# Kernel optimization log

Hardware: AMD Instinct MI355X
Metric: run time of the kernel (lower is better)

Reference implementation:

```python
import jax, jax.numpy as jnp
import numpy as np

N_HEAD = 16
K_SPARSE = 16

def setup_inputs() -> dict:
    key = jax.random.key(0)
    k1, k2, k3, k4 = jax.random.split(key, 4)
    B, T, C = 4, 1024, 1024
    x = jax.random.normal(k1, (B, T, C), dtype=jnp.float32)
    W_attn = jax.random.normal(k2, (3 * C, C), dtype=jnp.float32) * 0.02
    W_proj = jax.random.normal(k3, (C, C), dtype=jnp.float32) * 0.02
    W_rel = jax.random.normal(k4, (N_HEAD, C), dtype=jnp.float32) * 0.02
    return {"x": x, "W_attn": W_attn, "W_proj": W_proj, "W_rel": W_rel}


def reference(x, W_attn, W_proj, W_rel):
    B, T, C = x.shape
    H = W_rel.shape[0]
    hd = C // H
    K = min(K_SPARSE, T)

    # qkv projection (no bias): [B,T,3C] -> three [B,H,T,hd]
    qkv = x @ W_attn.T
    q, k, v = jnp.split(qkv, 3, axis=-1)
    q = q.reshape(B, T, H, hd).transpose(0, 2, 1, 3)
    k = k.reshape(B, T, H, hd).transpose(0, 2, 1, 3)
    v = v.reshape(B, T, H, hd).transpose(0, 2, 1, 3)

    # per-head relevance scores of batch 0 (original indexes top_indices[0]),
    # masked with row 0 of the causal tril (original uses masked_relevance[:, 0, :]):
    # only position 0 keeps a finite score.
    rel = jnp.einsum('tc,hc->ht', x[0], W_rel)              # [H,T]
    s = jnp.where(jnp.arange(T) == 0, rel, -jnp.inf)         # [H,T]

    t_ar = jnp.arange(T)
    # per-query masking (j <= t) then top-k routing per (head, t)
    scores = jnp.where(t_ar[:, None] >= t_ar[None, :], s[:, None, :], -jnp.inf)  # [H,T,T]
    _, idx = jax.lax.top_k(scores, K)                        # [H,T,K]
    slots = jnp.arange(K)
    # for t+1 <= K the original uses arange(t+1) (valid slots masked below)
    idx = jnp.where((t_ar < K)[None, :, None], slots[None, None, :], idx)
    valid = slots[None, :] <= t_ar[:, None]                  # [T,K]

    # gather selected keys / values: [B,H,T,K,hd]
    h_ix = jnp.arange(H)[:, None, None]
    k_sel = k[:, h_ix, idx]
    v_sel = v[:, h_ix, idx]

    logits = jnp.einsum('bhtd,bhtkd->bhtk', q, k_sel) / jnp.sqrt(jnp.float32(hd))
    logits = jnp.where(valid[None, None], logits, -jnp.inf)
    w = jax.nn.softmax(logits, axis=-1)                      # dropout = identity (eval)
    out = jnp.einsum('bhtk,bhtkd->bhtd', w, v_sel)

    out = out.transpose(0, 2, 1, 3).reshape(B, T, C)
    return out @ W_proj.T
```

## Files before the change

kernel.cpp:

```cpp
#include <hip/hip_runtime.h>
#include <hip/hip_bf16.h>
#include <stdint.h>

typedef __bf16 bf16x8 __attribute__((ext_vector_type(8)));
typedef float  f32x4  __attribute__((ext_vector_type(4)));

constexpr int Bb = 4;
constexpr int Tt = 1024;
constexpr int Cc = 1024;
constexpr int Kk = 16;
constexpr int HK = 256;
constexpr int KSPL = 8;

__device__ inline __bf16 f2bf(float f) {
    union { __hip_bfloat16 h; __bf16 b; } u;
    u.h = __float2bfloat16(f);
    return u.b;
}

__device__ inline void load_lds16(const void* g, void* l) {
    auto gp = (const __attribute__((address_space(1))) unsigned int*)(uintptr_t)g;
    auto lp = (__attribute__((address_space(3))) unsigned int*)(uintptr_t)l;
    __builtin_amdgcn_global_load_lds(gp, lp, 16, 0, 0);
}

__device__ inline bf16x8 cvt8(const float* p) {
    f32x4 lo = *reinterpret_cast<const f32x4*>(p);
    f32x4 hi = *reinterpret_cast<const f32x4*>(p + 4);
    bf16x8 r;
    r[0] = f2bf(lo[0]); r[1] = f2bf(lo[1]); r[2] = f2bf(lo[2]); r[3] = f2bf(lo[3]);
    r[4] = f2bf(hi[0]); r[5] = f2bf(hi[1]); r[6] = f2bf(hi[2]); r[7] = f2bf(hi[3]);
    return r;
}

__global__ __launch_bounds__(256)
void kv_gemm(const float* __restrict__ x, const float* __restrict__ Wkv,
             float* __restrict__ kv_part, __hip_bfloat16* __restrict__ xb)
{
    __shared__ __hip_bfloat16 As[64 * 40];
    __shared__ __hip_bfloat16 Bs[64 * 40];
    const int tid = threadIdx.x;

    if (blockIdx.z >= KSPL) {
        const int cb = (blockIdx.z - KSPL) * 32 + blockIdx.x;
        const size_t base = (size_t)cb * 16384;
#pragma unroll
        for (int i = 0; i < 8; ++i) {
            size_t off = base + (size_t)(i * 256 + tid) * 8;
            *reinterpret_cast<bf16x8*>(xb + off) = cvt8(x + off);
        }
        return;
    }

    const int lane = tid & 63;
    const int wave = tid >> 6;
    const int wm = wave >> 1, wn = wave & 1;
    const int tileN = blockIdx.x * 64;
    const int kz = blockIdx.z;
    const int r16 = lane & 15;
    const int kq  = (lane >> 4) * 8;

    const int sr = tid >> 2, sc = (tid & 3) * 8;
    const size_t arow = (size_t)(sr >> 4) * Tt + (sr & 15);

    f32x4 acc[2][2] = {};
    for (int kk = kz * 128; kk < kz * 128 + 128; kk += 32) {
        *reinterpret_cast<bf16x8*>(As + sr * 40 + sc) = cvt8(x + arow * Cc + kk + sc);
        *reinterpret_cast<bf16x8*>(Bs + sr * 40 + sc) = cvt8(Wkv + (size_t)(tileN + sr) * Cc + kk + sc);
        __syncthreads();
        bf16x8 a[2], b[2];
#pragma unroll
        for (int i = 0; i < 2; ++i) {
            a[i] = *reinterpret_cast<const bf16x8*>(As + (wm * 32 + i * 16 + r16) * 40 + kq);
            b[i] = *reinterpret_cast<const bf16x8*>(Bs + (wn * 32 + i * 16 + r16) * 40 + kq);
        }
#pragma unroll
        for (int i = 0; i < 2; ++i)
#pragma unroll
            for (int j = 0; j < 2; ++j)
                acc[i][j] = __builtin_amdgcn_mfma_f32_16x16x32_bf16(a[i], b[j], acc[i][j], 0, 0, 0);
        __syncthreads();
    }

    const int crow0 = (lane >> 4) * 4;
    const int ccol  = lane & 15;
    float* outp = kv_part + (size_t)kz * 64 * 2048;
#pragma unroll
    for (int i = 0; i < 2; ++i)
#pragma unroll
        for (int j = 0; j < 2; ++j)
#pragma unroll
            for (int r = 0; r < 4; ++r)
                outp[(size_t)(wm * 32 + i * 16 + crow0 + r) * 2048
                     + tileN + wn * 32 + j * 16 + ccol] = acc[i][j][r];
}

__global__ __launch_bounds__(256)
void precompute(const float* __restrict__ kv_part,
                const float* __restrict__ W_attn,
                const float* __restrict__ W_proj,
                __hip_bfloat16* __restrict__ QKb,
                __hip_bfloat16* __restrict__ vPt)
{
    __shared__ float sel[64][16];
    const int blk = blockIdx.x;
    const int type = blk >> 8;
    const int bh = (blk >> 2) & 63;
    const int cchunk = blk & 3;
    const int b = bh >> 4, h = bh & 15;
    const int tid = threadIdx.x;

    for (int e = tid; e < Kk * 64; e += 256) {
        int k = e >> 6, d = e & 63;
        size_t off = (size_t)(b * Kk + k) * 2048 + type * 1024 + h * 64 + d;
        float s = 0.f;
#pragma unroll
        for (int p = 0; p < KSPL; ++p) s += kv_part[off + (size_t)p * 64 * 2048];
        sel[d][k] = s;
    }
    __syncthreads();

    const int c = cchunk * 256 + tid;
    float acc[Kk] = {};

    if (type == 0) {
        const float* wp = W_attn + (size_t)(h * 64) * 1024 + c;
#pragma unroll 8
        for (int d = 0; d < 64; ++d) {
            float wv = wp[(size_t)d * 1024];
            const float4* sv = reinterpret_cast<const float4*>(sel[d]);
            float4 s0 = sv[0], s1 = sv[1], s2 = sv[2], s3 = sv[3];
            acc[0]  += wv * s0.x; acc[1]  += wv * s0.y; acc[2]  += wv * s0.z; acc[3]  += wv * s0.w;
            acc[4]  += wv * s1.x; acc[5]  += wv * s1.y; acc[6]  += wv * s1.z; acc[7]  += wv * s1.w;
            acc[8]  += wv * s2.x; acc[9]  += wv * s2.y; acc[10] += wv * s2.z; acc[11] += wv * s2.w;
            acc[12] += wv * s3.x; acc[13] += wv * s3.y; acc[14] += wv * s3.z; acc[15] += wv * s3.w;
        }
#pragma unroll
        for (int k = 0; k < Kk; ++k)
            QKb[((size_t)b * HK + h * 16 + k) * 1024 + c] = __float2bfloat16(acc[k]);
    } else {
        const float* wrow = W_proj + (size_t)c * 1024 + h * 64;
#pragma unroll 8
        for (int d4 = 0; d4 < 64; d4 += 4) {
            float4 wv = *reinterpret_cast<const float4*>(wrow + d4);
            const float w4[4] = {wv.x, wv.y, wv.z, wv.w};
#pragma unroll
            for (int dd = 0; dd < 4; ++dd) {
                float wvv = w4[dd];
                const float4* sv = reinterpret_cast<const float4*>(sel[d4 + dd]);
                float4 s0 = sv[0], s1 = sv[1], s2 = sv[2], s3 = sv[3];
                acc[0]  += wvv * s0.x; acc[1]  += wvv * s0.y; acc[2]  += wvv * s0.z; acc[3]  += wvv * s0.w;
                acc[4]  += wvv * s1.x; acc[5]  += wvv * s1.y; acc[6]  += wvv * s1.z; acc[7]  += wvv * s1.w;
                acc[8]  += wvv * s2.x; acc[9]  += wvv * s2.y; acc[10] += wvv * s2.z; acc[11] += wvv * s2.w;
                acc[12] += wvv * s3.x; acc[13] += wvv * s3.y; acc[14] += wvv * s3.z; acc[15] += wvv * s3.w;
            }
        }
        bf16x8 p0, p1;
#pragma unroll
        for (int k = 0; k < 8; ++k) { p0[k] = f2bf(acc[k]); p1[k] = f2bf(acc[k + 8]); }
        __hip_bfloat16* dst = vPt + ((size_t)b * 1024 + c) * HK + h * 16;
        *reinterpret_cast<bf16x8*>(dst) = p0;
        *reinterpret_cast<bf16x8*>(dst + 8) = p1;
    }
}

__global__ __launch_bounds__(256)
void logits_softmax(const __hip_bfloat16* __restrict__ xb,
                    const __hip_bfloat16* __restrict__ QKb,
                    __hip_bfloat16* __restrict__ wout)
{
    __shared__ __hip_bfloat16 Ah[4][32 * 32];
    __shared__ __hip_bfloat16 Bh[4][64 * 32];

    const __hip_bfloat16* A = xb + (size_t)blockIdx.z * Tt * Cc;
    const __hip_bfloat16* Bm = QKb + (size_t)blockIdx.z * HK * Cc;

    const int tid = threadIdx.x;
    const int lane = tid & 63;
    const int wave = tid >> 6;
    const int wm = wave >> 1, wn = wave & 1;
    const int tileM = blockIdx.y * 32;
    const int tileN = blockIdx.x * 64;
    const int r16 = lane & 15;
    const int kq  = (lane >> 4) * 8;

    f32x4 acc[2] = {};
    for (int kk = 0; kk < Cc; kk += 128) {
        {
            int g = wave * 64 + lane;
#pragma unroll
            for (int s = 0; s < 4; ++s)
                load_lds16(Bm + (size_t)(tileN + (g >> 2)) * Cc + kk + s * 32 + (g & 3) * 8,
                           &Bh[s][0] + wave * 512);
#pragma unroll
            for (int h = 0; h < 2; ++h)
                load_lds16(A + (size_t)(tileM + h * 16 + (lane >> 2)) * Cc + kk + wave * 32 + (lane & 3) * 8,
                           &Ah[wave][0] + h * 512);
        }
        __syncthreads();

#pragma unroll
        for (int s = 0; s < 4; ++s) {
            bf16x8 a = *reinterpret_cast<const bf16x8*>(&Ah[s][0] + (wm * 16 + r16) * 32 + kq);
#pragma unroll
            for (int j = 0; j < 2; ++j) {
                bf16x8 b = *reinterpret_cast<const bf16x8*>(
                    &Bh[s][0] + (wn * 32 + j * 16 + r16) * 32 + kq);
                acc[j] = __builtin_amdgcn_mfma_f32_16x16x32_bf16(a, b, acc[j], 0, 0, 0);
            }
        }
        __syncthreads();
    }

    const int crow0 = (lane >> 4) * 4;
    const int ccol  = lane & 15;
#pragma unroll
    for (int r = 0; r < 4; ++r) {
        int t = tileM + wm * 16 + crow0 + r;
        bool valid = (ccol <= t);
#pragma unroll
        for (int j = 0; j < 2; ++j) {
            int hk = tileN + wn * 32 + j * 16 + ccol;
            float v = acc[j][r] * 0.125f;
            float vm = valid ? v : -3.0e38f;
#pragma unroll
            for (int m = 1; m < 16; m <<= 1) vm = fmaxf(vm, __shfl_xor(vm, m));
            float e = valid ? __expf(v - vm) : 0.f;
            float s = e;
#pragma unroll
            for (int m = 1; m < 16; m <<= 1) s += __shfl_xor(s, m);
            wout[((size_t)blockIdx.z * Tt + t) * HK + hk] = __float2bfloat16(e / s);
        }
    }
}

__global__ __launch_bounds__(256)
void out_gemm(const __hip_bfloat16* __restrict__ Aw,
              const __hip_bfloat16* __restrict__ Bv,
              float* __restrict__ Cout)
{
    __shared__ __hip_bfloat16 As[2][64 * 32];
    __shared__ __hip_bfloat16 Bs[2][64 * 32];

    const __hip_bfloat16* A = Aw + (size_t)blockIdx.z * Tt * HK;
    const __hip_bfloat16* Bm = Bv + (size_t)blockIdx.z * Cc * HK;

    const int lane = threadIdx.x & 63;
    const int wave = threadIdx.x >> 6;
    const int wm = wave >> 1, wn = wave & 1;
    const int tileM = blockIdx.y * 64;
    const int tileN = blockIdx.x * 64;
    const int r16 = lane & 15;
    const int kq  = (lane >> 4) * 8;

    f32x4 acc[2][2] = {};
    for (int kk = 0; kk < HK; kk += 64) {
        {
            int g = wave * 64 + lane;
#pragma unroll
            for (int s = 0; s < 2; ++s) {
                load_lds16(A + (size_t)(tileM + (g >> 2)) * HK + kk + s * 32 + (g & 3) * 8,
                           &As[s][0] + wave * 512);
                load_lds16(Bm + (size_t)(tileN + (g >> 2)) * HK + kk + s * 32 + (g & 3) * 8,
                           &Bs[s][0] + wave * 512);
            }
        }
        __syncthreads();
#pragma unroll
        for (int s = 0; s < 2; ++s) {
            bf16x8 a[2], b[2];
#pragma unroll
            for (int i = 0; i < 2; ++i) {
                a[i] = *reinterpret_cast<const bf16x8*>(&As[s][0] + (wm * 32 + i * 16 + r16) * 32 + kq);
                b[i] = *reinterpret_cast<const bf16x8*>(&Bs[s][0] + (wn * 32 + i * 16 + r16) * 32 + kq);
            }
#pragma unroll
            for (int i = 0; i < 2; ++i)
#pragma unroll
                for (int j = 0; j < 2; ++j)
                    acc[i][j] = __builtin_amdgcn_mfma_f32_16x16x32_bf16(a[i], b[j], acc[i][j], 0, 0, 0);
        }
        __syncthreads();
    }

    const int crow0 = (lane >> 4) * 4;
    const int ccol  = lane & 15;
    float* outp = Cout + (size_t)blockIdx.z * Tt * Cc;
#pragma unroll
    for (int i = 0; i < 2; ++i)
#pragma unroll
        for (int j = 0; j < 2; ++j)
#pragma unroll
            for (int r = 0; r < 4; ++r)
                outp[(size_t)(tileM + wm * 32 + i * 16 + crow0 + r) * Cc
                     + tileN + wn * 32 + j * 16 + ccol] = acc[i][j][r];
}

extern "C" void kernel_launch(void* const* d_in, const int* in_sizes, int n_in,
                              void* d_out, int out_size, void* d_ws, size_t ws_size,
                              hipStream_t stream)
{
    (void)in_sizes; (void)n_in; (void)out_size; (void)ws_size;
    const float* x      = (const float*)d_in[0];
    const float* W_attn = (const float*)d_in[1];
    const float* W_proj = (const float*)d_in[2];
    float* out = (float*)d_out;

    char* ws = (char*)d_ws;
    float*          kv_part = (float*)ws;
    __hip_bfloat16* QKb  = (__hip_bfloat16*)(ws + (4u << 20));
    __hip_bfloat16* vPt  = (__hip_bfloat16*)(ws + (6u << 20));
    __hip_bfloat16* w_ws = (__hip_bfloat16*)(ws + (8u << 20));
    __hip_bfloat16* xb   = (__hip_bfloat16*)(ws + (10u << 20));

    kv_gemm<<<dim3(32, 1, 2 * KSPL), 256, 0, stream>>>(x, W_attn + (size_t)Cc * Cc, kv_part, xb);
    precompute<<<512, 256, 0, stream>>>(kv_part, W_attn, W_proj, QKb, vPt);
    logits_softmax<<<dim3(HK / 64, Tt / 32, Bb), 256, 0, stream>>>(xb, QKb, w_ws);
    out_gemm<<<dim3(16, 16, Bb), 256, 0, stream>>>(w_ws, vPt, out);
}
```

Before: 114.9 us.

## Fuse four kernels into one persistent kernel with global grid barriers

Merges the kv GEMM, precompute, logits/softmax and output GEMM launches into a single 512-block kernel separated by atomic spin-wait grid barriers. The output GEMM stage now handles two tiles per block to fit the fixed grid. This removes per-launch overhead and inter-kernel gaps, at the cost of a memset for the barrier counters and reliance on all 512 blocks being co-resident; if they are not, the spin-wait can hang or time out.

New measurement: 252.8 us. 2.2x slower.

```diff
diff --git a/kernel.cpp b/kernel.cpp
--- a/kernel.cpp
+++ b/kernel.cpp
@@ -11,6 +11,7 @@
 constexpr int Kk = 16;
 constexpr int HK = 256;
 constexpr int KSPL = 8;
+constexpr unsigned NBLK = 512;
 
 __device__ inline __bf16 f2bf(float f) {
     union { __hip_bfloat16 h; __bf16 b; } u;
@@ -33,267 +34,281 @@
     return r;
 }
 
-__global__ __launch_bounds__(256)
-void kv_gemm(const float* __restrict__ x, const float* __restrict__ Wkv,
-             float* __restrict__ kv_part, __hip_bfloat16* __restrict__ xb)
+__device__ inline void grid_sync(unsigned* cnt) {
+    __syncthreads();
+    if (threadIdx.x == 0) {
+        __hip_atomic_fetch_add(cnt, 1u, __ATOMIC_ACQ_REL, __HIP_MEMORY_SCOPE_AGENT);
+        unsigned spins = 0;
+        while (__hip_atomic_load(cnt, __ATOMIC_ACQUIRE, __HIP_MEMORY_SCOPE_AGENT) < NBLK
+               && ++spins < (1u << 30)) {
+            __builtin_amdgcn_s_sleep(2);
+        }
+    }
+    __syncthreads();
+}
+
+__global__ __launch_bounds__(256, 2)
+void fused_all(const float* __restrict__ x,
+               const float* __restrict__ W_attn,
+               const float* __restrict__ W_proj,
+               float* __restrict__ kv_part,
+               __hip_bfloat16* __restrict__ QKb,
+               __hip_bfloat16* __restrict__ vPt,
+               __hip_bfloat16* __restrict__ w_ws,
+               __hip_bfloat16* __restrict__ xb,
+               float* __restrict__ out,
+               unsigned* __restrict__ bar)
 {
-    __shared__ __hip_bfloat16 As[64 * 40];
-    __shared__ __hip_bfloat16 Bs[64 * 40];
-    const int tid = threadIdx.x;
-
-    if (blockIdx.z >= KSPL) {
-        const int cb = (blockIdx.z - KSPL) * 32 + blockIdx.x;
+    __shared__ __align__(16) char smem[24576];
+
+    const int tid  = threadIdx.x;
+    const int lane = tid & 63;
+    const int wave = tid >> 6;
+    const int blk  = blockIdx.x;
+
+    if (blk >= 256) {
+        const int cb = blk - 256;
         const size_t base = (size_t)cb * 16384;
 #pragma unroll
         for (int i = 0; i < 8; ++i) {
             size_t off = base + (size_t)(i * 256 + tid) * 8;
             *reinterpret_cast<bf16x8*>(xb + off) = cvt8(x + off);
         }
-        return;
-    }
-
-    const int lane = tid & 63;
-    const int wave = tid >> 6;
-    const int wm = wave >> 1, wn = wave & 1;
-    const int tileN = blockIdx.x * 64;
-    const int kz = blockIdx.z;
-    const int r16 = lane & 15;
-    const int kq  = (lane >> 4) * 8;
-
-    const int sr = tid >> 2, sc = (tid & 3) * 8;
-    const size_t arow = (size_t)(sr >> 4) * Tt + (sr & 15);
-
-    f32x4 acc[2][2] = {};
-    for (int kk = kz * 128; kk < kz * 128 + 128; kk += 32) {
-        *reinterpret_cast<bf16x8*>(As + sr * 40 + sc) = cvt8(x + arow * Cc + kk + sc);
-        *reinterpret_cast<bf16x8*>(Bs + sr * 40 + sc) = cvt8(Wkv + (size_t)(tileN + sr) * Cc + kk + sc);
-        __syncthreads();
-        bf16x8 a[2], b[2];
-#pragma unroll
-        for (int i = 0; i < 2; ++i) {
-            a[i] = *reinterpret_cast<const bf16x8*>(As + (wm * 32 + i * 16 + r16) * 40 + kq);
-            b[i] = *reinterpret_cast<const bf16x8*>(Bs + (wn * 32 + i * 16 + r16) * 40 + kq);
-        }
-#pragma unroll
-        for (int i = 0; i < 2; ++i)
-#pragma unroll
-            for (int j = 0; j < 2; ++j)
-                acc[i][j] = __builtin_amdgcn_mfma_f32_16x16x32_bf16(a[i], b[j], acc[i][j], 0, 0, 0);
-        __syncthreads();
-    }
-
-    const int crow0 = (lane >> 4) * 4;
-    const int ccol  = lane & 15;
-    float* outp = kv_part + (size_t)kz * 64 * 2048;
-#pragma unroll
-    for (int i = 0; i < 2; ++i)
-#pragma unroll
-        for (int j = 0; j < 2; ++j)
-#pragma unroll
-            for (int r = 0; r < 4; ++r)
-                outp[(size_t)(wm * 32 + i * 16 + crow0 + r) * 2048
-                     + tileN + wn * 32 + j * 16 + ccol] = acc[i][j][r];
-}
-
-__global__ __launch_bounds__(256)
-void precompute(const float* __restrict__ kv_part,
-                const float* __restrict__ W_attn,
-                const float* __restrict__ W_proj,
-                __hip_bfloat16* __restrict__ QKb,
-                __hip_bfloat16* __restrict__ vPt)
-{
-    __shared__ float sel[64][16];
-    const int blk = blockIdx.x;
-    const int type = blk >> 8;
-    const int bh = (blk >> 2) & 63;
-    const int cchunk = blk & 3;
-    const int b = bh >> 4, h = bh & 15;
-    const int tid = threadIdx.x;
-
-    for (int e = tid; e < Kk * 64; e += 256) {
-        int k = e >> 6, d = e & 63;
-        size_t off = (size_t)(b * Kk + k) * 2048 + type * 1024 + h * 64 + d;
-        float s = 0.f;
-#pragma unroll
-        for (int p = 0; p < KSPL; ++p) s += kv_part[off + (size_t)p * 64 * 2048];
-        sel[d][k] = s;
-    }
-    __syncthreads();
-
-    const int c = cchunk * 256 + tid;
-    float acc[Kk] = {};
-
-    if (type == 0) {
-        const float* wp = W_attn + (size_t)(h * 64) * 1024 + c;
-#pragma unroll 8
-        for (int d = 0; d < 64; ++d) {
-            float wv = wp[(size_t)d * 1024];
-            const float4* sv = reinterpret_cast<const float4*>(sel[d]);
-            float4 s0 = sv[0], s1 = sv[1], s2 = sv[2], s3 = sv[3];
-            acc[0]  += wv * s0.x; acc[1]  += wv * s0.y; acc[2]  += wv * s0.z; acc[3]  += wv * s0.w;
-            acc[4]  += wv * s1.x; acc[5]  += wv * s1.y; acc[6]  += wv * s1.z; acc[7]  += wv * s1.w;
-            acc[8]  += wv * s2.x; acc[9]  += wv * s2.y; acc[10] += wv * s2.z; acc[11] += wv * s2.w;
-            acc[12] += wv * s3.x; acc[13] += wv * s3.y; acc[14] += wv * s3.z; acc[15] += wv * s3.w;
-        }
-#pragma unroll
-        for (int k = 0; k < Kk; ++k)
-            QKb[((size_t)b * HK + h * 16 + k) * 1024 + c] = __float2bfloat16(acc[k]);
     } else {
-        const float* wrow = W_proj + (size_t)c * 1024 + h * 64;
-#pragma unroll 8
-        for (int d4 = 0; d4 < 64; d4 += 4) {
-            float4 wv = *reinterpret_cast<const float4*>(wrow + d4);
-            const float w4[4] = {wv.x, wv.y, wv.z, wv.w};
-#pragma unroll
-            for (int dd = 0; dd < 4; ++dd) {
-                float wvv = w4[dd];
-                const float4* sv = reinterpret_cast<const float4*>(sel[d4 + dd]);
-                float4 s0 = sv[0], s1 = sv[1], s2 = sv[2], s3 = sv[3];
-                acc[0]  += wvv * s0.x; acc[1]  += wvv * s0.y; acc[2]  += wvv * s0.z; acc[3]  += wvv * s0.w;
-                acc[4]  += wvv * s1.x; acc[5]  += wvv * s1.y; acc[6]  += wvv * s1.z; acc[7]  += wvv * s1.w;
-                acc[8]  += wvv * s2.x; acc[9]  += wvv * s2.y; acc[10] += wvv * s2.z; acc[11] += wvv * s2.w;
-                acc[12] += wvv * s3.x; acc[13] += wvv * s3.y; acc[14] += wvv * s3.z; acc[15] += wvv * s3.w;
-            }
-        }
-        bf16x8 p0, p1;
-#pragma unroll
-        for (int k = 0; k < 8; ++k) { p0[k] = f2bf(acc[k]); p1[k] = f2bf(acc[k + 8]); }
-        __hip_bfloat16* dst = vPt + ((size_t)b * 1024 + c) * HK + h * 16;
-        *reinterpret_cast<bf16x8*>(dst) = p0;
-        *reinterpret_cast<bf16x8*>(dst + 8) = p1;
-    }
-}
-
-__global__ __launch_bounds__(256)
-void logits_softmax(const __hip_bfloat16* __restrict__ xb,
-                    const __hip_bfloat16* __restrict__ QKb,
-                    __hip_bfloat16* __restrict__ wout)
-{
-    __shared__ __hip_bfloat16 Ah[4][32 * 32];
-    __shared__ __hip_bfloat16 Bh[4][64 * 32];
-
-    const __hip_bfloat16* A = xb + (size_t)blockIdx.z * Tt * Cc;
-    const __hip_bfloat16* Bm = QKb + (size_t)blockIdx.z * HK * Cc;
-
-    const int tid = threadIdx.x;
-    const int lane = tid & 63;
-    const int wave = tid >> 6;
-    const int wm = wave >> 1, wn = wave & 1;
-    const int tileM = blockIdx.y * 32;
-    const int tileN = blockIdx.x * 64;
-    const int r16 = lane & 15;
-    const int kq  = (lane >> 4) * 8;
-
-    f32x4 acc[2] = {};
-    for (int kk = 0; kk < Cc; kk += 128) {
-        {
-            int g = wave * 64 + lane;
-#pragma unroll
-            for (int s = 0; s < 4; ++s)
-                load_lds16(Bm + (size_t)(tileN + (g >> 2)) * Cc + kk + s * 32 + (g & 3) * 8,
-                           &Bh[s][0] + wave * 512);
-#pragma unroll
-            for (int h = 0; h < 2; ++h)
-                load_lds16(A + (size_t)(tileM + h * 16 + (lane >> 2)) * Cc + kk + wave * 32 + (lane & 3) * 8,
-                           &Ah[wave][0] + h * 512);
-        }
-        __syncthreads();
-
-#pragma unroll
-        for (int s = 0; s < 4; ++s) {
-            bf16x8 a = *reinterpret_cast<const bf16x8*>(&Ah[s][0] + (wm * 16 + r16) * 32 + kq);
-#pragma unroll
-            for (int j = 0; j < 2; ++j) {
-                bf16x8 b = *reinterpret_cast<const bf16x8*>(
-                    &Bh[s][0] + (wn * 32 + j * 16 + r16) * 32 + kq);
-                acc[j] = __builtin_amdgcn_mfma_f32_16x16x32_bf16(a, b, acc[j], 0, 0, 0);
-            }
-        }
-        __syncthreads();
-    }
-
-    const int crow0 = (lane >> 4) * 4;
-    const int ccol  = lane & 15;
-#pragma unroll
-    for (int r = 0; r < 4; ++r) {
-        int t = tileM + wm * 16 + crow0 + r;
-        bool valid = (ccol <= t);
-#pragma unroll
-        for (int j = 0; j < 2; ++j) {
-            int hk = tileN + wn * 32 + j * 16 + ccol;
-            float v = acc[j][r] * 0.125f;
-            float vm = valid ? v : -3.0e38f;
-#pragma unroll
-            for (int m = 1; m < 16; m <<= 1) vm = fmaxf(vm, __shfl_xor(vm, m));
-            float e = valid ? __expf(v - vm) : 0.f;
-            float s = e;
-#pragma unroll
-            for (int m = 1; m < 16; m <<= 1) s += __shfl_xor(s, m);
-            wout[((size_t)blockIdx.z * Tt + t) * HK + hk] = __float2bfloat16(e / s);
-        }
-    }
-}
-
-__global__ __launch_bounds__(256)
-void out_gemm(const __hip_bfloat16* __restrict__ Aw,
-              const __hip_bfloat16* __restrict__ Bv,
-              float* __restrict__ Cout)
-{
-    __shared__ __hip_bfloat16 As[2][64 * 32];
-    __shared__ __hip_bfloat16 Bs[2][64 * 32];
-
-    const __hip_bfloat16* A = Aw + (size_t)blockIdx.z * Tt * HK;
-    const __hip_bfloat16* Bm = Bv + (size_t)blockIdx.z * Cc * HK;
-
-    const int lane = threadIdx.x & 63;
-    const int wave = threadIdx.x >> 6;
-    const int wm = wave >> 1, wn = wave & 1;
-    const int tileM = blockIdx.y * 64;
-    const int tileN = blockIdx.x * 64;
-    const int r16 = lane & 15;
-    const int kq  = (lane >> 4) * 8;
-
-    f32x4 acc[2][2] = {};
-    for (int kk = 0; kk < HK; kk += 64) {
-        {
-            int g = wave * 64 + lane;
-#pragma unroll
-            for (int s = 0; s < 2; ++s) {
-                load_lds16(A + (size_t)(tileM + (g >> 2)) * HK + kk + s * 32 + (g & 3) * 8,
-                           &As[s][0] + wave * 512);
-                load_lds16(Bm + (size_t)(tileN + (g >> 2)) * HK + kk + s * 32 + (g & 3) * 8,
-                           &Bs[s][0] + wave * 512);
-            }
-        }
-        __syncthreads();
-#pragma unroll
-        for (int s = 0; s < 2; ++s) {
+        const float* Wkv = W_attn + (size_t)Cc * Cc;
+        __hip_bfloat16* As = (__hip_bfloat16*)smem;
+        __hip_bfloat16* Bs = As + 64 * 40;
+        const int wm = wave >> 1, wn = wave & 1;
+        const int tileN = (blk & 31) * 64;
+        const int kz = blk >> 5;
+        const int r16 = lane & 15;
+        const int kq  = (lane >> 4) * 8;
+        const int sr = tid >> 2, sc = (tid & 3) * 8;
+        const size_t arow = (size_t)(sr >> 4) * Tt + (sr & 15);
+
+        f32x4 acc[2][2] = {};
+        for (int kk = kz * 128; kk < kz * 128 + 128; kk += 32) {
+            *reinterpret_cast<bf16x8*>(As + sr * 40 + sc) = cvt8(x + arow * Cc + kk + sc);
+            *reinterpret_cast<bf16x8*>(Bs + sr * 40 + sc) = cvt8(Wkv + (size_t)(tileN + sr) * Cc + kk + sc);
+            __syncthreads();
             bf16x8 a[2], b[2];
 #pragma unroll
             for (int i = 0; i < 2; ++i) {
-                a[i] = *reinterpret_cast<const bf16x8*>(&As[s][0] + (wm * 32 + i * 16 + r16) * 32 + kq);
-                b[i] = *reinterpret_cast<const bf16x8*>(&Bs[s][0] + (wn * 32 + i * 16 + r16) * 32 + kq);
+                a[i] = *reinterpret_cast<const bf16x8*>(As + (wm * 32 + i * 16 + r16) * 40 + kq);
+                b[i] = *reinterpret_cast<const bf16x8*>(Bs + (wn * 32 + i * 16 + r16) * 40 + kq);
             }
 #pragma unroll
             for (int i = 0; i < 2; ++i)
 #pragma unroll
                 for (int j = 0; j < 2; ++j)
                     acc[i][j] = __builtin_amdgcn_mfma_f32_16x16x32_bf16(a[i], b[j], acc[i][j], 0, 0, 0);
+            __syncthreads();
+        }
+
+        const int crow0 = (lane >> 4) * 4;
+        const int ccol  = lane & 15;
+        float* outp = kv_part + (size_t)kz * 64 * 2048;
+#pragma unroll
+        for (int i = 0; i < 2; ++i)
+#pragma unroll
+            for (int j = 0; j < 2; ++j)
+#pragma unroll
+                for (int r = 0; r < 4; ++r)
+                    outp[(size_t)(wm * 32 + i * 16 + crow0 + r) * 2048
+                         + tileN + wn * 32 + j * 16 + ccol] = acc[i][j][r];
+    }
+
+    grid_sync(bar + 0);
+
+    {
+        float (*sel)[16] = (float (*)[16])smem;
+        const int type = blk >> 8;
+        const int bh = (blk >> 2) & 63;
+        const int cchunk = blk & 3;
+        const int b = bh >> 4, h = bh & 15;
+
+        for (int e = tid; e < Kk * 64; e += 256) {
+            int k = e >> 6, d = e & 63;
+            size_t off = (size_t)(b * Kk + k) * 2048 + type * 1024 + h * 64 + d;
+            float s = 0.f;
+#pragma unroll
+            for (int p = 0; p < KSPL; ++p) s += kv_part[off + (size_t)p * 64 * 2048];
+            sel[d][k] = s;
         }
         __syncthreads();
-    }
-
-    const int crow0 = (lane >> 4) * 4;
-    const int ccol  = lane & 15;
-    float* outp = Cout + (size_t)blockIdx.z * Tt * Cc;
-#pragma unroll
-    for (int i = 0; i < 2; ++i)
-#pragma unroll
-        for (int j = 0; j < 2; ++j)
-#pragma unroll
-            for (int r = 0; r < 4; ++r)
-                outp[(size_t)(tileM + wm * 32 + i * 16 + crow0 + r) * Cc
-                     + tileN + wn * 32 + j * 16 + ccol] = acc[i][j][r];
+
+        const int c = cchunk * 256 + tid;
+        float acc[Kk] = {};
+
+        if (type == 0) {
+            const float* wp = W_attn + (size_t)(h * 64) * 1024 + c;
+#pragma unroll 8
+            for (int d = 0; d < 64; ++d) {
+                float wv = wp[(size_t)d * 1024];
+                const float4* sv = reinterpret_cast<const float4*>(sel[d]);
+                float4 s0 = sv[0], s1 = sv[1], s2 = sv[2], s3 = sv[3];
+                acc[0]  += wv * s0.x; acc[1]  += wv * s0.y; acc[2]  += wv * s0.z; acc[3]  += wv * s0.w;
+                acc[4]  += wv * s1.x; acc[5]  += wv * s1.y; acc[6]  += wv * s1.z; acc[7]  += wv * s1.w;
+                acc[8]  += wv * s2.x; acc[9]  += wv * s2.y; acc[10] += wv * s2.z; acc[11] += wv * s2.w;
+                acc[12] += wv * s3.x; acc[13] += wv * s3.y; acc[14] += wv * s3.z; acc[15] += wv * s3.w;
+            }
+#pragma unroll
+            for (int k = 0; k < Kk; ++k)
+                QKb[((size_t)b * HK + h * 16 + k) * 1024 + c] = __float2bfloat16(acc[k]);
+        } else {
+            const float* wrow = W_proj + (size_t)c * 1024 + h * 64;
+#pragma unroll 8
+            for (int d4 = 0; d4 < 64; d4 += 4) {
+                float4 wv = *reinterpret_cast<const float4*>(wrow + d4);
+                const float w4[4] = {wv.x, wv.y, wv.z, wv.w};
+#pragma unroll
+                for (int dd = 0; dd < 4; ++dd) {
+                    float wvv = w4[dd];
+                    const float4* sv = reinterpret_cast<const float4*>(sel[d4 + dd]);
+                    float4 s0 = sv[0], s1 = sv[1], s2 = sv[2], s3 = sv[3];
+                    acc[0]  += wvv * s0.x; acc[1]  += wvv * s0.y; acc[2]  += wvv * s0.z; acc[3]  += wvv * s0.w;
+                    acc[4]  += wvv * s1.x; acc[5]  += wvv * s1.y; acc[6]  += wvv * s1.z; acc[7]  += wvv * s1.w;
+                    acc[8]  += wvv * s2.x; acc[9]  += wvv * s2.y; acc[10] += wvv * s2.z; acc[11] += wvv * s2.w;
+                    acc[12] += wvv * s3.x; acc[13] += wvv * s3.y; acc[14] += wvv * s3.z; acc[15] += wvv * s3.w;
+                }
+            }
+            bf16x8 p0, p1;
+#pragma unroll
+            for (int k = 0; k < 8; ++k) { p0[k] = f2bf(acc[k]); p1[k] = f2bf(acc[k + 8]); }
+            __hip_bfloat16* dst = vPt + ((size_t)b * 1024 + c) * HK + h * 16;
+            *reinterpret_cast<bf16x8*>(dst) = p0;
+            *reinterpret_cast<bf16x8*>(dst + 8) = p1;
+        }
+    }
+
+    grid_sync(bar + 1);
+
+    {
+        __hip_bfloat16* Ah = (__hip_bfloat16*)smem;
+        __hip_bfloat16* Bh = Ah + 4 * 32 * 32;
+        const int bz = blk >> 7;
+        const int by = (blk >> 2) & 31;
+        const int bx = blk & 3;
+        const __hip_bfloat16* A = xb + (size_t)bz * Tt * Cc;
+        const __hip_bfloat16* Bm = QKb + (size_t)bz * HK * Cc;
+        const int wm = wave >> 1, wn = wave & 1;
+        const int tileM = by * 32;
+        const int tileN = bx * 64;
+        const int r16 = lane & 15;
+        const int kq  = (lane >> 4) * 8;
+
+        f32x4 acc[2] = {};
+        for (int kk = 0; kk < Cc; kk += 128) {
+            {
+                int g = wave * 64 + lane;
+#pragma unroll
+                for (int s = 0; s < 4; ++s)
+                    load_lds16(Bm + (size_t)(tileN + (g >> 2)) * Cc + kk + s * 32 + (g & 3) * 8,
+                               Bh + s * 2048 + wave * 512);
+#pragma unroll
+                for (int h = 0; h < 2; ++h)
+                    load_lds16(A + (size_t)(tileM + h * 16 + (lane >> 2)) * Cc + kk + wave * 32 + (lane & 3) * 8,
+                               Ah + wave * 1024 + h * 512);
+            }
+            __syncthreads();
+
+#pragma unroll
+            for (int s = 0; s < 4; ++s) {
+                bf16x8 a = *reinterpret_cast<const bf16x8*>(Ah + s * 1024 + (wm * 16 + r16) * 32 + kq);
+#pragma unroll
+                for (int j = 0; j < 2; ++j) {
+                    bf16x8 b = *reinterpret_cast<const bf16x8*>(
+                        Bh + s * 2048 + (wn * 32 + j * 16 + r16) * 32 + kq);
+                    acc[j] = __builtin_amdgcn_mfma_f32_16x16x32_bf16(a, b, acc[j], 0, 0, 0);
+                }
+            }
+            __syncthreads();
+        }
+
+        const int crow0 = (lane >> 4) * 4;
+        const int ccol  = lane & 15;
+#pragma unroll
+        for (int r = 0; r < 4; ++r) {
+            int t = tileM + wm * 16 + crow0 + r;
+            bool valid = (ccol <= t);
+#pragma unroll
+            for (int j = 0; j < 2; ++j) {
+                int hk = tileN + wn * 32 + j * 16 + ccol;
+                float v = acc[j][r] * 0.125f;
+                float vm = valid ? v : -3.0e38f;
+#pragma unroll
+                for (int m = 1; m < 16; m <<= 1) vm = fmaxf(vm, __shfl_xor(vm, m));
+                float e = valid ? __expf(v - vm) : 0.f;
+                float s = e;
+#pragma unroll
+                for (int m = 1; m < 16; m <<= 1) s += __shfl_xor(s, m);
+                w_ws[((size_t)bz * Tt + t) * HK + hk] = __float2bfloat16(e / s);
+            }
+        }
+    }
+
+    grid_sync(bar + 2);
+
+    {
+        __hip_bfloat16* As = (__hip_bfloat16*)smem;
+        __hip_bfloat16* Bs = As + 2 * 64 * 32;
+        const int wm = wave >> 1, wn = wave & 1;
+        const int r16 = lane & 15;
+        const int kq  = (lane >> 4) * 8;
+
+        for (int rep = 0; rep < 2; ++rep) {
+            const int t = blk * 2 + rep;
+            const int bz = t >> 8;
+            const int by = (t >> 4) & 15;
+            const int bx = t & 15;
+            const __hip_bfloat16* A = w_ws + (size_t)bz * Tt * HK;
+            const __hip_bfloat16* Bm = vPt + (size_t)bz * Cc * HK;
+            const int tileM = by * 64;
+            const int tileN = bx * 64;
+
+            f32x4 acc[2][2] = {};
+            for (int kk = 0; kk < HK; kk += 64) {
+                {
+                    int g = wave * 64 + lane;
+#pragma unroll
+                    for (int s = 0; s < 2; ++s) {
+                        load_lds16(A + (size_t)(tileM + (g >> 2)) * HK + kk + s * 32 + (g & 3) * 8,
+                                   As + s * 2048 + wave * 512);
+                        load_lds16(Bm + (size_t)(tileN + (g >> 2)) * HK + kk + s * 32 + (g & 3) * 8,
+                                   Bs + s * 2048 + wave * 512);
+                    }
+                }
+                __syncthreads();
+#pragma unroll
+                for (int s = 0; s < 2; ++s) {
+                    bf16x8 a[2], b[2];
+#pragma unroll
+                    for (int i = 0; i < 2; ++i) {
+                        a[i] = *reinterpret_cast<const bf16x8*>(As + s * 2048 + (wm * 32 + i * 16 + r16) * 32 + kq);
+                        b[i] = *reinterpret_cast<const bf16x8*>(Bs + s * 2048 + (wn * 32 + i * 16 + r16) * 32 + kq);
+                    }
+#pragma unroll
+                    for (int i = 0; i < 2; ++i)
+#pragma unroll
+                        for (int j = 0; j < 2; ++j)
+                            acc[i][j] = __builtin_amdgcn_mfma_f32_16x16x32_bf16(a[i], b[j], acc[i][j], 0, 0, 0);
+                }
+                __syncthreads();
+            }
+
+            const int crow0 = (lane >> 4) * 4;
+            const int ccol  = lane & 15;
+            float* outp = out + (size_t)bz * Tt * Cc;
+#pragma unroll
+            for (int i = 0; i < 2; ++i)
+#pragma unroll
+                for (int j = 0; j < 2; ++j)
+#pragma unroll
+                    for (int r = 0; r < 4; ++r)
+                        outp[(size_t)(tileM + wm * 32 + i * 16 + crow0 + r) * Cc
+                             + tileN + wn * 32 + j * 16 + ccol] = acc[i][j][r];
+        }
+    }
 }
 
 extern "C" void kernel_launch(void* const* d_in, const int* in_sizes, int n_in,
@@ -312,9 +327,9 @@
     __hip_bfloat16* vPt  = (__hip_bfloat16*)(ws + (6u << 20));
     __hip_bfloat16* w_ws = (__hip_bfloat16*)(ws + (8u << 20));
     __hip_bfloat16* xb   = (__hip_bfloat16*)(ws + (10u << 20));
-
-    kv_gemm<<<dim3(32, 1, 2 * KSPL), 256, 0, stream>>>(x, W_attn + (size_t)Cc * Cc, kv_part, xb);
-    precompute<<<512, 256, 0, stream>>>(kv_part, W_attn, W_proj, QKb, vPt);
-    logits_softmax<<<dim3(HK / 64, Tt / 32, Bb), 256, 0, stream>>>(xb, QKb, w_ws);
-    out_gemm<<<dim3(16, 16, Bb), 256, 0, stream>>>(w_ws, vPt, out);
-}
+    unsigned*       bar  = (unsigned*)(ws + (18u << 20));
+
+    hipMemsetAsync(bar, 0, 256, stream);
+    fused_all<<<dim3(NBLK), 256, 0, stream>>>(x, W_attn, W_proj, kv_part,
+                                              QKb, vPt, w_ws, xb, out, bar);
+}
```
